# Kernel tuning notes

Hardware: AMD Instinct MI355X
Metric: run time of the kernel (lower is better)

Reference implementation:

```python
import jax
import jax.numpy as jnp
import numpy as np

KSIZE, STRIDE, RATE, FUSE_K, SCALE = 3, 1, 2, 3, 10.0
ESCAPE_NAN = 1e-4


def _same_pad(x, k, s):
    # replicates torch same_padding: asymmetric zero pad so out = ceil(H/s)
    H, W = x.shape[2], x.shape[3]
    oh, ow = -(-H // s), -(-W // s)
    ph = max(0, (oh - 1) * s + k - H)
    pw = max(0, (ow - 1) * s + k - W)
    return jnp.pad(x, ((0, 0), (0, 0), (ph // 2, ph - ph // 2), (pw // 2, pw - pw // 2)))


def _extract_patches(x, k, s):
    # torch extract_image_patches: -> [B, L, C, k, k] with L = out_h*out_w
    x = _same_pad(x, k, s)
    B, C, H, W = x.shape
    Ho, Wo = (H - k) // s + 1, (W - k) // s + 1
    slices = [x[:, :, i:i + Ho * s:s, j:j + Wo * s:s] for i in range(k) for j in range(k)]
    p = jnp.stack(slices, axis=2).reshape(B, C, k, k, Ho, Wo)
    return p.transpose(0, 4, 5, 1, 2, 3).reshape(B, Ho * Wo, C, k, k)


def _contextual_attention(f, b, mask):
    dn = ('NCHW', 'OIHW', 'NCHW')
    # raw background patches for the final deconv: k = 2*rate, stride = rate
    raw_pat = _extract_patches(b, 2 * RATE, RATE * STRIDE)  # [B, L, C, 4, 4]
    # nearest-neighbor 1/rate downsample (torch F.interpolate nearest, sf=0.5)
    f_ds = f[:, :, ::RATE, ::RATE]
    b_ds = b[:, :, ::RATE, ::RATE]
    m_ds = mask[:, :, ::RATE, ::RATE]
    B, C, Hf, Wf = f_ds.shape
    Hb, Wb = b_ds.shape[2], b_ds.shape[3]
    b_pat = _extract_patches(b_ds, KSIZE, STRIDE)  # [B, L, C, 3, 3], L = Hb*Wb
    m_pat = _extract_patches(m_ds, KSIZE, STRIDE)[0]  # [L, 1, 3, 3] (first sample only, as in torch)
    mm = (jnp.mean(m_pat, axis=(1, 2, 3)) == 0.0).astype(f.dtype)[None, :, None, None]  # [1, L, 1, 1]
    fuse_w = jnp.eye(FUSE_K, dtype=f.dtype).reshape(1, 1, FUSE_K, FUSE_K)

    def per_item(xi, wi, raw_wi):
        # xi: [C,Hf,Wf]; wi: [L,C,3,3]; raw_wi: [L,C,4,4]
        max_wi = jnp.sqrt(jnp.sum(wi * wi + ESCAPE_NAN, axis=(1, 2, 3), keepdims=True))
        wi_n = wi / max_wi
        # matching conv: scores [1, L, Hf, Wf]
        yi = jax.lax.conv_general_dilated(xi[None], wi_n, (1, 1), ((1, 1), (1, 1)), dimension_numbers=dn)
        # fuse: identity-diagonal 3x3 conv along (bg_idx, fg_idx) twice with transposes
        yi = yi.reshape(1, 1, Hb * Wb, Hf * Wf)
        yi = jax.lax.conv_general_dilated(yi, fuse_w, (1, 1), ((1, 1), (1, 1)), dimension_numbers=dn)
        yi = yi.reshape(Hb, Wb, Hf, Wf).transpose(1, 0, 3, 2).reshape(1, 1, Hb * Wb, Hf * Wf)
        yi = jax.lax.conv_general_dilated(yi, fuse_w, (1, 1), ((1, 1), (1, 1)), dimension_numbers=dn)
        yi = yi.reshape(Wb, Hb, Wf, Hf).transpose(1, 0, 3, 2).reshape(1, Hb * Wb, Hf, Wf)
        yi = yi * mm
        yi = jax.nn.softmax(yi * SCALE, axis=1) * mm
        # conv_transpose2d(yi, raw_wi[I=L,O=C], stride=rate, padding=1) / 4
        w2 = jnp.flip(raw_wi, (2, 3)).transpose(1, 0, 2, 3)  # [C, L, 4, 4]
        pad = 2 * RATE - 1 - 1  # k - 1 - torch_padding = 2
        out = jax.lax.conv_general_dilated(yi, w2, (1, 1), ((pad, pad), (pad, pad)),
                                           lhs_dilation=(RATE, RATE), dimension_numbers=dn) / 4.0
        return out[0]

    return jax.vmap(per_item)(f_ds, b_pat, raw_pat)  # [B, C, H, W]


def setup_inputs() -> dict:
    key = jax.random.key(0)
    k1, k2 = jax.random.split(key)
    B, C, H, W = 2, 128, 128, 128
    f = jax.random.normal(k1, (B, C, H, W), dtype=jnp.float32)
    b = jax.random.normal(k2, (B, C, H, W), dtype=jnp.float32)
    mask = jnp.zeros((B, 1, H, W), dtype=jnp.float32)
    return {"f": f, "b": b, "mask": mask}


def reference(f, b, mask):
    return _contextual_attention(f, b, mask)
```

## Files before the change

kernel.cpp:

```cpp
#include <hip/hip_runtime.h>
#include <math.h>

#define CDIM 128
#define HF   128
#define WF   128
#define NP   4096
#define NCHUNK 64

typedef __attribute__((ext_vector_type(8))) short short8;
typedef __attribute__((ext_vector_type(16))) float f16a;
typedef float __attribute__((ext_vector_type(4), aligned(16))) f4a16;
typedef float __attribute__((ext_vector_type(4), aligned(4)))  f4u;

__device__ inline ushort f2bf(float x) {
  union { float f; unsigned u; } v; v.f = x;
  unsigned r = v.u + 0x7fff + ((v.u >> 16) & 1);
  return (ushort)(r >> 16);
}
__device__ inline float bf2f(ushort h) {
  union { unsigned u; float f; } v; v.u = ((unsigned)h) << 16; return v.f;
}

__device__ inline void gl2lds16(const ushort* g, ushort* l) {
  __builtin_amdgcn_global_load_lds((const __attribute__((address_space(1))) void*)g,
                                   (__attribute__((address_space(3))) void*)l, 16, 0, 0);
}

__global__ __launch_bounds__(256) void k_prep(const float* __restrict__ f,
                                              const float* __restrict__ b,
                                              ushort* __restrict__ fcat,
                                              ushort* __restrict__ bcat,
                                              float* __restrict__ s2) {
  int idx = blockIdx.x * 256 + threadIdx.x;
  int c = idx & 127, pos = idx >> 7;
  int x = pos & 63, y = pos >> 6;
  int src = c * 16384 + y * 256 + x * 2;
  float fv = f[src], bv = b[src];
  ushort fh = f2bf(fv); ushort fl = f2bf(fv - bf2f(fh));
  ushort bh = f2bf(bv); ushort bl = f2bf(bv - bf2f(bh));
  size_t base = (size_t)pos * 384;
  fcat[base + c] = fh; fcat[base + 128 + c] = fl; fcat[base + 256 + c] = fh;
  bcat[base + c] = bh; bcat[base + 128 + c] = bh; bcat[base + 256 + c] = bl;
  float sq = bv * bv;
#pragma unroll
  for (int off = 32; off; off >>= 1) sq += __shfl_down(sq, off);
  __shared__ float wsum[4];
  if ((threadIdx.x & 63) == 0) wsum[threadIdx.x >> 6] = sq;
  __syncthreads();
  if (threadIdx.x == 0) s2[blockIdx.x * 2]     = wsum[0] + wsum[1];
  if (threadIdx.x == 1) s2[blockIdx.x * 2 + 1] = wsum[2] + wsum[3];
}

__global__ __launch_bounds__(256) void k_mmpnorm(const float* __restrict__ mask,
                                                 const float* __restrict__ s2,
                                                 float* __restrict__ mmp,
                                                 float* __restrict__ rnrm) {
  int bx = blockIdx.x, t = threadIdx.x;
  if (bx < 16) {
    int a = bx * 256 + t;
    int yb = a & 63, xb = a >> 6;
    float s = 0.f;
    for (int dy = -1; dy <= 1; ++dy)
      for (int dx = -1; dx <= 1; ++dx) {
        int y = yb + dy, x = xb + dx;
        if ((unsigned)y < 64u && (unsigned)x < 64u)
          s += mask[y * 256 + x * 2];
      }
    mmp[a] = (s == 0.0f) ? 1.0f : 0.0f;
  } else {
    int p = (bx - 16) * 256 + t;
    int xb = p & 63, yb = p >> 6;
    float s = 0.f;
    for (int dy = -1; dy <= 1; ++dy)
      for (int dx = -1; dx <= 1; ++dx) {
        int y = yb + dy, x = xb + dx;
        if ((unsigned)y < 64u && (unsigned)x < 64u) s += s2[y * 64 + x];
      }
    rnrm[p] = rsqrtf(s + 1152.0f * 1.0e-4f);
  }
}

__global__ __launch_bounds__(256) void k_mfma_gemm(const ushort* __restrict__ A,
                                                   const ushort* __restrict__ B,
                                                   float* __restrict__ Out,
                                                   int Kdim, int lda, int ldb, int ldo) {
  __shared__ ushort As[128 * 64];
  __shared__ ushort Bs[128 * 64];
  int tid = threadIdx.x;
  int wave = tid >> 6, lane = tid & 63;
  int l32 = lane & 31, khalf = lane >> 5;
  int m0 = blockIdx.y * 128, n0 = blockIdx.x * 128;
  int wm = (wave >> 1) * 64, wn = (wave & 1) * 64;
  int srow = lane >> 3;
  int g = lane & 7;
  int gperm = (g ^ srow) * 8;

  f16a acc[2][2];
#pragma unroll
  for (int i = 0; i < 2; ++i)
#pragma unroll
    for (int j = 0; j < 2; ++j)
#pragma unroll
      for (int r = 0; r < 16; ++r) acc[i][j][r] = 0.f;

  for (int k0 = 0; k0 < Kdim; k0 += 64) {
#pragma unroll
    for (int i = 0; i < 4; ++i) {
      int rbase = wave * 32 + i * 8;
      gl2lds16(A + (size_t)(m0 + rbase + srow) * lda + k0 + gperm, &As[rbase * 64]);
      gl2lds16(B + (size_t)(n0 + rbase + srow) * ldb + k0 + gperm, &Bs[rbase * 64]);
    }
    __syncthreads();
#pragma unroll
    for (int s = 0; s < 4; ++s) {
      short8 af[2], bf[2];
#pragma unroll
      for (int t2 = 0; t2 < 2; ++t2) {
        int am = wm + t2 * 32 + l32;
        int ga = ((s * 2 + khalf) ^ (am & 7)) * 8;
        af[t2] = *reinterpret_cast<const short8*>(&As[am * 64 + ga]);
        int bn = wn + t2 * 32 + l32;
        int gb = ((s * 2 + khalf) ^ (bn & 7)) * 8;
        bf[t2] = *reinterpret_cast<const short8*>(&Bs[bn * 64 + gb]);
      }
#pragma unroll
      for (int i = 0; i < 2; ++i)
#pragma unroll
        for (int j = 0; j < 2; ++j)
          acc[i][j] = __builtin_amdgcn_mfma_f32_32x32x16_bf16(af[i], bf[j], acc[i][j], 0, 0, 0);
    }
    __syncthreads();
  }
#pragma unroll
  for (int i = 0; i < 2; ++i)
#pragma unroll
    for (int j = 0; j < 2; ++j)
#pragma unroll
      for (int r = 0; r < 16; ++r) {
        int row = (r & 3) + 8 * (r >> 2) + 4 * khalf;
        Out[(size_t)(m0 + wm + i * 32 + row) * ldo + (n0 + wn + j * 32 + l32)] = acc[i][j][r];
      }
}

__global__ __launch_bounds__(256) void k_s0(const float* __restrict__ D,
                                            const float* __restrict__ rnrm,
                                            float* __restrict__ S0) {
  int p = blockIdx.x;
  int yb = p >> 6, xb = p & 63;
  float rp = rnrm[p];
  int t = threadIdx.x;
#pragma unroll
  for (int it = 0; it < 4; ++it) {
    int q = (it * 256 + t) << 2;
    int qy = q >> 6, qx = q & 63;
    f4a16 acc = (f4a16){0.f, 0.f, 0.f, 0.f};
#pragma unroll
    for (int dy = -1; dy <= 1; ++dy) {
      if ((unsigned)(yb + dy) >= 64u) continue;
      if ((unsigned)(qy + dy) >= 64u) continue;
#pragma unroll
      for (int dx = -1; dx <= 1; ++dx) {
        if ((unsigned)(xb + dx) >= 64u) continue;
        int delta = dy * 64 + dx;
        const float* base = D + (size_t)(p + delta) * 4096;
        f4u v;
        if (dx == -1 && qx == 0) {
          f4u r = *(const f4u*)(base + q + delta + 1);
          v = (f4u){0.f, r.x, r.y, r.z};
        } else {
          v = *(const f4u*)(base + q + delta);
          if (dx == 1 && qx == 60) v.w = 0.f;
        }
        acc += v;
      }
    }
    acc *= rp;
    *(f4a16*)(S0 + ((size_t)p << 12) + q) = acc;
  }
}

__global__ __launch_bounds__(256) void k_fuse1(const float* __restrict__ S0,
                                               float* __restrict__ Yp) {
  __shared__ float row[4160];
  int i = blockIdx.x;
  int t = threadIdx.x;
  const float* r0 = S0 + (size_t)(i - 1) * 4096;
  const float* r1 = S0 + (size_t)i * 4096;
  const float* r2 = S0 + (size_t)(i + 1) * 4096;
  bool up = (i > 0), dn = (i < 4095);
#pragma unroll
  for (int jj = 0; jj < 4; ++jj) {
    int j = (jj * 256 + t) << 2;
    f4u s = *(const f4u*)(r1 + j);
    if (up) {
      f4u a;
      if (j == 0) { f4u r = *(const f4u*)r0; a = (f4u){0.f, r.x, r.y, r.z}; }
      else a = *(const f4u*)(r0 + j - 1);
      s += a;
    }
    if (dn) {
      f4u d = *(const f4u*)(r2 + j + 1);
      if (j == 4092) d.w = 0.f;
      s += d;
    }
    int base = j + (j >> 6);
    row[base + 0] = s.x; row[base + 1] = s.y; row[base + 2] = s.z; row[base + 3] = s.w;
  }
  __syncthreads();
  int a = ((i & 63) << 6) | (i >> 6);
  float* orow = Yp + ((size_t)a << 12);
#pragma unroll
  for (int bb = 0; bb < 4; ++bb) {
    int b4 = (bb * 256 + t) << 2;
    f4a16 o;
#pragma unroll
    for (int k = 0; k < 4; ++k) {
      int jT = (((b4 + k) & 63) << 6) | ((b4 + k) >> 6);
      o[k] = row[jT + (jT >> 6)];
    }
    *(f4a16*)(orow + b4) = o;
  }
}

__global__ __launch_bounds__(256) void k_smax_part(const float* __restrict__ Yp,
                                                   const float* __restrict__ mmp,
                                                   float* __restrict__ pm,
                                                   float* __restrict__ ps) {
  int v = (blockIdx.x * 256 + threadIdx.x) << 2;
  int chunk = blockIdx.y;
  f4a16 m = (f4a16){-1e30f, -1e30f, -1e30f, -1e30f};
  f4a16 s = (f4a16){0.f, 0.f, 0.f, 0.f};
  int u0 = chunk * (4096 / NCHUNK);
  for (int u = u0; u < u0 + (4096 / NCHUNK); ++u) {
    const float* row = Yp + ((size_t)u << 12);
    f4u tv = *(const f4u*)(row + v);
    if (u > 0) {
      f4u a;
      if (v == 0) { f4u r = *(const f4u*)(row - 4096); a = (f4u){0.f, r.x, r.y, r.z}; }
      else a = *(const f4u*)(row - 4096 + v - 1);
      tv += a;
    }
    if (u < 4095) {
      f4u d = *(const f4u*)(row + 4096 + v + 1);
      if (v == 4092) d.w = 0.f;
      tv += d;
    }
    float g = 10.0f * mmp[u];
    f4u x = tv * g;
#pragma unroll
    for (int l = 0; l < 4; ++l) {
      float xl = x[l];
      if (xl > m[l]) { s[l] = s[l] * __expf(m[l] - xl) + 1.0f; m[l] = xl; }
      else           { s[l] += __expf(xl - m[l]); }
    }
  }
  *(f4a16*)(pm + chunk * NP + v) = m;
  *(f4a16*)(ps + chunk * NP + v) = s;
}

__global__ __launch_bounds__(256) void k_epilogue(const float* __restrict__ Yp,
                                                  const float* __restrict__ pm,
                                                  const float* __restrict__ ps,
                                                  const float* __restrict__ mmp,
                                                  ushort* __restrict__ AT,
                                                  const float* __restrict__ bimg,
                                                  ushort* __restrict__ VtT) {
  __shared__ float T[64][65];
  __shared__ float pmS[4][64];
  __shared__ float psS[4][64];
  __shared__ float mS[64];
  __shared__ float rsS[64];
  int gx = blockIdx.x;
  int t = threadIdx.x;
  if (gx < 4096) {
    int a0 = (gx & 63) * 64, b0 = (gx >> 6) * 64;
    int j = t & 63, grp = t >> 6;
    float m = -1e30f, s = 0.f;
    for (int ch = grp * 16; ch < grp * 16 + 16; ++ch) {
      float m2 = pm[ch * NP + b0 + j], s2 = ps[ch * NP + b0 + j];
      if (m2 > m) { s = s * __expf(m - m2) + s2; m = m2; }
      else        { s += s2 * __expf(m2 - m); }
    }
    pmS[grp][j] = m; psS[grp][j] = s;
    __syncthreads();
    if (grp == 0) {
      for (int g2 = 1; g2 < 4; ++g2) {
        float m2 = pmS[g2][j], s2 = psS[g2][j];
        if (m2 > m) { s = s * __expf(m - m2) + s2; m = m2; }
        else        { s += s2 * __expf(m2 - m); }
      }
      mS[j] = m; rsS[j] = 1.0f / s;
    }
    __syncthreads();
    int i = t >> 4, j4 = (t & 15) << 2;
    f4a16 mc = *(const f4a16*)&mS[j4];
    f4a16 rs = *(const f4a16*)&rsS[j4];
#pragma unroll
    for (int r = 0; r < 4; ++r) {
      int al = r * 16 + i;
      int a = a0 + al;
      const float* row = Yp + ((size_t)a << 12);
      int b = b0 + j4;
      f4u y = *(const f4u*)(row + b);
      if (a > 0) {
        f4u u_;
        if (b == 0) { f4u rr = *(const f4u*)(row - 4096); u_ = (f4u){0.f, rr.x, rr.y, rr.z}; }
        else u_ = *(const f4u*)(row - 4096 + b - 1);
        y += u_;
      }
      if (a < 4095) {
        f4u d = *(const f4u*)(row + 4096 + b + 1);
        if (b == 4092) d.w = 0.f;
        y += d;
      }
      float g = mmp[a];
      f4u x = y * (10.0f * g);
#pragma unroll
      for (int l = 0; l < 4; ++l)
        T[al][j4 + l] = g * __expf(x[l] - mc[l]) * rs[l];
    }
    __syncthreads();
    int by0 = b0 >> 6;
    int cgrp = (t & 7) * 8;
#pragma unroll
    for (int pass = 0; pass < 2; ++pass) {
      int bl = pass * 32 + (t >> 3);
      int q = bl * 64 + by0;
      uint4 w;
      w.x = (unsigned)f2bf(T[cgrp + 0][bl]) | ((unsigned)f2bf(T[cgrp + 1][bl]) << 16);
      w.y = (unsigned)f2bf(T[cgrp + 2][bl]) | ((unsigned)f2bf(T[cgrp + 3][bl]) << 16);
      w.z = (unsigned)f2bf(T[cgrp + 4][bl]) | ((unsigned)f2bf(T[cgrp + 5][bl]) << 16);
      w.w = (unsigned)f2bf(T[cgrp + 6][bl]) | ((unsigned)f2bf(T[cgrp + 7][bl]) << 16);
      *(uint4*)(AT + ((size_t)q << 12) + a0 + cgrp) = w;
    }
  } else {
    int k2 = gx - 4096;
    int c = k2 >> 4, dy = (k2 >> 2) & 3, dx = k2 & 3;
    int px = t & 63;
#pragma unroll
    for (int r = 0; r < 16; ++r) {
      int py = r * 4 + (t >> 6);
      int sy = 2 * py + dy - 1, sx = 2 * px + dx - 1;
      float v = 0.f;
      if ((unsigned)sy < (unsigned)HF && (unsigned)sx < (unsigned)WF)
        v = bimg[c * 16384 + sy * 128 + sx];
      T[py][px] = v;
    }
    __syncthreads();
    ushort* orow = VtT + (size_t)k2 * 4096;
#pragma unroll
    for (int r = 0; r < 16; ++r) {
      int a = r * 256 + t;
      orow[a] = f2bf(T[a & 63][a >> 6]);
    }
  }
}

__global__ __launch_bounds__(256) void k_scatter(const float* __restrict__ M,
                                                 float* __restrict__ out) {
  int idx = blockIdx.x * 256 + threadIdx.x;
  int ox = idx & 127, oy = (idx >> 7) & 127, c = idx >> 14;
  int qy[2], dyv[2], qx[2], dxv[2];
  if (oy & 1) { qy[0] = (oy - 1) >> 1; dyv[0] = 2; qy[1] = (oy + 1) >> 1; dyv[1] = 0; }
  else        { qy[0] = (oy >> 1) - 1; dyv[0] = 3; qy[1] = oy >> 1;       dyv[1] = 1; }
  if (ox & 1) { qx[0] = (ox - 1) >> 1; dxv[0] = 2; qx[1] = (ox + 1) >> 1; dxv[1] = 0; }
  else        { qx[0] = (ox >> 1) - 1; dxv[0] = 3; qx[1] = ox >> 1;       dxv[1] = 1; }
  float s = 0.f;
#pragma unroll
  for (int i = 0; i < 2; ++i) {
    if ((unsigned)qy[i] >= 64u) continue;
#pragma unroll
    for (int j = 0; j < 2; ++j) {
      if ((unsigned)qx[j] >= 64u) continue;
      int k = c * 16 + dyv[i] * 4 + dxv[j];
      s += M[(size_t)k * NP + qy[i] * 64 + qx[j]];
    }
  }
  out[idx] = 0.25f * s;
}

extern "C" void kernel_launch(void* const* d_in, const int* in_sizes, int n_in,
                              void* d_out, int out_size, void* d_ws, size_t ws_size,
                              hipStream_t stream) {
  const float* f_all = (const float*)d_in[0];
  const float* b_all = (const float*)d_in[1];
  const float* m_all = (const float*)d_in[2];
  float* out = (float*)d_out;

  float* ws = (float*)d_ws;
  float* bufD = ws;
  float* bufS = ws + 16777216;
  ushort* fcat = (ushort*)bufS;
  ushort* bcat = (ushort*)(bufS + 786432);
  float* S0  = bufS;
  float* Yp  = bufD;
  ushort* AT  = (ushort*)bufS;
  ushort* VtT = (ushort*)(bufS + 8388608);
  float* Mbuf = bufD;
  float* smalls = ws + 2 * 16777216;
  float* s2    = smalls;
  float* rnrm  = s2 + 4096;
  float* mmp   = rnrm + 4096;
  float* pm    = mmp + 4096;
  float* ps    = pm + NCHUNK * NP;

  const size_t zsF = (size_t)CDIM * HF * WF;
  const size_t zsM = (size_t)HF * WF;

  for (int it = 0; it < 2; ++it) {
    const float* f = f_all + it * zsF;
    const float* b = b_all + it * zsF;
    const float* mk = m_all + it * zsM;
    float* o = out + it * zsF;

    k_prep<<<2048, 256, 0, stream>>>(f, b, fcat, bcat, s2);
    k_mmpnorm<<<32, 256, 0, stream>>>(mk, s2, mmp, rnrm);
    k_mfma_gemm<<<dim3(32, 32), 256, 0, stream>>>(bcat, fcat, bufD, 384, 384, 384, NP);
    k_s0<<<4096, 256, 0, stream>>>(bufD, rnrm, S0);
    k_fuse1<<<4096, 256, 0, stream>>>(S0, Yp);
    k_smax_part<<<dim3(4, NCHUNK), 256, 0, stream>>>(Yp, mmp, pm, ps);
    k_epilogue<<<6144, 256, 0, stream>>>(Yp, pm, ps, mmp, AT, b, VtT);
    k_mfma_gemm<<<dim3(32, 16), 256, 0, stream>>>(VtT, AT, Mbuf, NP, NP, NP, NP);
    k_scatter<<<8192, 256, 0, stream>>>(Mbuf, o);
  }
}
```

Before: 668.4 us.

## Triple-buffer LDS in MFMA GEMM with 256x128 tiles and 8 waves

The bf16 MFMA GEMM moves from a 128x128 tile with 4 waves to a 256x128 tile with 8 waves. K-tiles are staged into LDS through three rotating buffers, two tiles ahead, using direct global-to-LDS loads. The global loads are split across two half-steps and guarded by explicit vmcnt/lgkmcnt waits, split barriers and s_setprio around the MFMA bursts. The aim is to hide global load latency behind matrix math, replacing the load, sync, compute, sync pattern. In exchange it uses more LDS per block (about 144KB) and half as many blocks, which may hurt occupancy or wave count on the smaller first GEMM.

```diff
diff --git a/kernel.cpp b/kernel.cpp
--- a/kernel.cpp
+++ b/kernel.cpp
@@ -80,20 +80,29 @@
   }
 }
 
-__global__ __launch_bounds__(256) void k_mfma_gemm(const ushort* __restrict__ A,
+__global__ __launch_bounds__(512) void k_mfma_gemm(const ushort* __restrict__ A,
                                                    const ushort* __restrict__ B,
                                                    float* __restrict__ Out,
                                                    int Kdim, int lda, int ldb, int ldo) {
-  __shared__ ushort As[128 * 64];
-  __shared__ ushort Bs[128 * 64];
-  int tid = threadIdx.x;
-  int wave = tid >> 6, lane = tid & 63;
-  int l32 = lane & 31, khalf = lane >> 5;
-  int m0 = blockIdx.y * 128, n0 = blockIdx.x * 128;
-  int wm = (wave >> 1) * 64, wn = (wave & 1) * 64;
-  int srow = lane >> 3;
-  int g = lane & 7;
-  int gperm = (g ^ srow) * 8;
+  __shared__ ushort As[3][256 * 64];
+  __shared__ ushort Bs[3][128 * 64];
+  const int tid = threadIdx.x;
+  const int wave = tid >> 6, lane = tid & 63;
+  const int l32 = lane & 31, khalf = lane >> 5;
+  const int m0 = blockIdx.y * 256, n0 = blockIdx.x * 128;
+  const int wm = (wave >> 1) * 64, wn = (wave & 1) * 64;
+  const int srow = lane >> 3;
+  const int gperm = ((lane & 7) ^ srow) * 8;
+
+  const ushort* Ag = A + (size_t)(m0 + wave * 8 + srow) * lda + gperm;
+  const ushort* Bg = B + (size_t)(n0 + wave * 8 + srow) * ldb + gperm;
+  ushort* AsW = &As[0][0] + (wave * 8) * 64;
+  ushort* BsW = &Bs[0][0] + (wave * 8) * 64;
+
+#define STG_A(bufi, tt, q) gl2lds16(Ag + (size_t)((q) * 64) * lda + ((tt) << 6), \
+                                    AsW + (bufi) * 16384 + (q) * 4096)
+#define STG_B(bufi, tt, q) gl2lds16(Bg + (size_t)((q) * 64) * ldb + ((tt) << 6), \
+                                    BsW + (bufi) * 8192 + (q) * 4096)
 
   f16a acc[2][2];
 #pragma unroll
@@ -103,34 +112,57 @@
 #pragma unroll
       for (int r = 0; r < 16; ++r) acc[i][j][r] = 0.f;
 
-  for (int k0 = 0; k0 < Kdim; k0 += 64) {
-#pragma unroll
-    for (int i = 0; i < 4; ++i) {
-      int rbase = wave * 32 + i * 8;
-      gl2lds16(A + (size_t)(m0 + rbase + srow) * lda + k0 + gperm, &As[rbase * 64]);
-      gl2lds16(B + (size_t)(n0 + rbase + srow) * ldb + k0 + gperm, &Bs[rbase * 64]);
-    }
-    __syncthreads();
-#pragma unroll
-    for (int s = 0; s < 4; ++s) {
-      short8 af[2], bf[2];
-#pragma unroll
-      for (int t2 = 0; t2 < 2; ++t2) {
-        int am = wm + t2 * 32 + l32;
-        int ga = ((s * 2 + khalf) ^ (am & 7)) * 8;
-        af[t2] = *reinterpret_cast<const short8*>(&As[am * 64 + ga]);
-        int bn = wn + t2 * 32 + l32;
-        int gb = ((s * 2 + khalf) ^ (bn & 7)) * 8;
-        bf[t2] = *reinterpret_cast<const short8*>(&Bs[bn * 64 + gb]);
-      }
-#pragma unroll
-      for (int i = 0; i < 2; ++i)
-#pragma unroll
-        for (int j = 0; j < 2; ++j)
-          acc[i][j] = __builtin_amdgcn_mfma_f32_32x32x16_bf16(af[i], bf[j], acc[i][j], 0, 0, 0);
-    }
-    __syncthreads();
-  }
+  const int NT = Kdim >> 6;
+
+  STG_A(0, 0, 0); STG_B(0, 0, 0); STG_A(0, 0, 1); STG_B(0, 0, 1); STG_A(0, 0, 2); STG_A(0, 0, 3);
+  STG_A(1, 1, 0); STG_B(1, 1, 0); STG_A(1, 1, 1); STG_B(1, 1, 1); STG_A(1, 1, 2); STG_A(1, 1, 3);
+  asm volatile("s_waitcnt vmcnt(6)");
+  __builtin_amdgcn_s_barrier();
+
+  int cb = 0, sb = 2;
+  for (int t = 0; t < NT; ++t) {
+    const ushort* Ar = &As[cb][0];
+    const ushort* Br = &Bs[cb][0];
+    const bool st = (t + 2) < NT;
+    const int tn = t + 2;
+#pragma unroll
+    for (int h = 0; h < 2; ++h) {
+      short8 af[2][2], bf[2][2];
+#pragma unroll
+      for (int ss = 0; ss < 2; ++ss) {
+        const int s = h * 2 + ss;
+#pragma unroll
+        for (int u = 0; u < 2; ++u) {
+          int am = wm + u * 32 + l32;
+          int ga = ((s * 2 + khalf) ^ (am & 7)) * 8;
+          af[ss][u] = *reinterpret_cast<const short8*>(&Ar[am * 64 + ga]);
+          int bn = wn + u * 32 + l32;
+          int gb = ((s * 2 + khalf) ^ (bn & 7)) * 8;
+          bf[ss][u] = *reinterpret_cast<const short8*>(&Br[bn * 64 + gb]);
+        }
+      }
+      if (st) {
+        if (h == 0) { STG_A(sb, tn, 0); STG_B(sb, tn, 0); STG_A(sb, tn, 1); }
+        else        { STG_B(sb, tn, 1); STG_A(sb, tn, 2); STG_A(sb, tn, 3); }
+      }
+      __builtin_amdgcn_s_barrier();
+      asm volatile("s_waitcnt lgkmcnt(0)");
+      __builtin_amdgcn_s_setprio(1);
+#pragma unroll
+      for (int ss = 0; ss < 2; ++ss) {
+        acc[0][0] = __builtin_amdgcn_mfma_f32_32x32x16_bf16(af[ss][0], bf[ss][0], acc[0][0], 0, 0, 0);
+        acc[0][1] = __builtin_amdgcn_mfma_f32_32x32x16_bf16(af[ss][0], bf[ss][1], acc[0][1], 0, 0, 0);
+        acc[1][0] = __builtin_amdgcn_mfma_f32_32x32x16_bf16(af[ss][1], bf[ss][0], acc[1][0], 0, 0, 0);
+        acc[1][1] = __builtin_amdgcn_mfma_f32_32x32x16_bf16(af[ss][1], bf[ss][1], acc[1][1], 0, 0, 0);
+      }
+      __builtin_amdgcn_s_setprio(0);
+      if (h == 1) asm volatile("s_waitcnt vmcnt(6)");
+      __builtin_amdgcn_s_barrier();
+    }
+    cb = (cb == 2) ? 0 : cb + 1;
+    sb = (sb == 2) ? 0 : sb + 1;
+  }
+
 #pragma unroll
   for (int i = 0; i < 2; ++i)
 #pragma unroll
@@ -140,6 +172,8 @@
         int row = (r & 3) + 8 * (r >> 2) + 4 * khalf;
         Out[(size_t)(m0 + wm + i * 32 + row) * ldo + (n0 + wn + j * 32 + l32)] = acc[i][j][r];
       }
+#undef STG_A
+#undef STG_B
 }
 
 __global__ __launch_bounds__(256) void k_s0(const float* __restrict__ D,
@@ -415,12 +449,12 @@
 
     k_prep<<<2048, 256, 0, stream>>>(f, b, fcat, bcat, s2);
     k_mmpnorm<<<32, 256, 0, stream>>>(mk, s2, mmp, rnrm);
-    k_mfma_gemm<<<dim3(32, 32), 256, 0, stream>>>(bcat, fcat, bufD, 384, 384, 384, NP);
+    k_mfma_gemm<<<dim3(32, 16), 512, 0, stream>>>(bcat, fcat, bufD, 384, 384, 384, NP);
     k_s0<<<4096, 256, 0, stream>>>(bufD, rnrm, S0);
     k_fuse1<<<4096, 256, 0, stream>>>(S0, Yp);
     k_smax_part<<<dim3(4, NCHUNK), 256, 0, stream>>>(Yp, mmp, pm, ps);
     k_epilogue<<<6144, 256, 0, stream>>>(Yp, pm, ps, mmp, AT, b, VtT);
-    k_mfma_gemm<<<dim3(32, 16), 256, 0, stream>>>(VtT, AT, Mbuf, NP, NP, NP, NP);
+    k_mfma_gemm<<<dim3(32, 8), 512, 0, stream>>>(VtT, AT, Mbuf, NP, NP, NP, NP);
     k_scatter<<<8192, 256, 0, stream>>>(Mbuf, o);
   }
 }
```

Result: no change. 669.6 us (+0.2%).
